# Optimization experiments

Measured on AMD Instinct MI355X. Metric: run time of the kernel, lower is better.

## Reference

```python
import jax, jax.numpy as jnp
import numpy as np
import math

V_RANGE = 1
SHIFTS = [(x, y) for x in range(-V_RANGE, V_RANGE + 1) for y in range(-V_RANGE, V_RANGE + 1)]


def circ_conv(x, w, b=None):
    # Conv2d with circular padding, NCHW / OIHW layout.
    p = w.shape[-1] // 2
    xp = jnp.pad(x, ((0, 0), (0, 0), (p, p), (p, p)), mode='wrap')
    y = jax.lax.conv_general_dilated(xp, w, (1, 1), 'VALID',
                                     dimension_numbers=('NCHW', 'OIHW', 'NCHW'))
    if b is not None:
        y = y + b[None, :, None, None]
    return y


def setup_inputs() -> dict:
    key = jax.random.key(0)
    ks = jax.random.split(key, 6)
    B, d_model, d_state, H, W = 4, 64, 16, 32, 32
    num_v = (2 * V_RANGE + 1) ** 2  # 9
    return {
        'u_t': jax.random.normal(ks[0], (B, d_model, H, W), jnp.float32),
        's_prev': jax.random.normal(ks[1], (B, num_v, d_model, d_state, H, W), jnp.float32),
        'W_delta': jax.random.normal(ks[2], (d_model, d_model, 3, 3), jnp.float32) * 0.05,
        'b_delta': jnp.zeros((d_model,), jnp.float32),
        'W_B': jax.random.normal(ks[3], (d_state, d_model, 3, 3), jnp.float32) * 0.05,
        'W_C': jax.random.normal(ks[4], (d_state, d_model, 3, 3), jnp.float32) * 0.05,
        'log_A_real': jnp.log(0.5 * jnp.ones((d_model, d_state), jnp.float32)),
        'D': jnp.ones((d_model,), jnp.float32),
        'dt_inv_softplus': jnp.float32(math.log(math.e - 1.0)),
    }


def reference(u_t, s_prev, W_delta, b_delta, W_B, W_C, log_A_real, D, dt_inv_softplus):
    # Parameter generation from input
    delta = jax.nn.softplus(circ_conv(u_t, W_delta, b_delta) + dt_inv_softplus)  # (B,d,H,W)
    B_val = circ_conv(u_t, W_B)  # (B,n,H,W)
    C_val = circ_conv(u_t, W_C)  # (B,n,H,W)

    # ZOH discretization (pointwise)
    A = -jnp.exp(log_A_real)                         # (d,n)
    A_bc = A[None, :, :, None, None]                 # (1,d,n,1,1)
    A_bar = jnp.exp(delta[:, :, None] * A_bc)        # (B,d,n,H,W)
    B_bar = (A_bar - 1.0) / A_bc * B_val[:, None]    # (B,d,n,H,W)
    bu = B_bar * u_t[:, :, None]                     # (B,d,n,H,W)

    # Transport: per-velocity spatial roll, vectorized with vmap over the V axis
    vx = jnp.array([s[0] for s in SHIFTS])
    vy = jnp.array([s[1] for s in SHIFTS])
    roll_v = jax.vmap(lambda s, x, y: jnp.roll(s, shift=(-y, -x), axis=(-2, -1)),
                      in_axes=(1, 0, 0), out_axes=1)
    s_trans = roll_v(s_prev, vx, vy)                 # (B,V,d,n,H,W)

    # State update and output
    s_next = A_bar[:, None] * s_trans + bu[:, None]  # (B,V,d,n,H,W)
    y_state = jnp.sum(s_next * C_val[:, None, None], axis=3)  # (B,V,d,H,W)
    y_out = y_state + (u_t * D[None, :, None, None])[:, None]
    return y_out, s_next
```

## Files before the change

kernel.cpp:

```cpp
#include <hip/hip_runtime.h>
#include <math.h>

#define B_   4
#define DM   64
#define DS   16
#define HW_  1024
#define NV   9

typedef float f32x4 __attribute__((ext_vector_type(4)));

#define Y_SIZE   2359296
#define WS_DELTA 0
#define WS_BV    (B_*DM*HW_)
#define WS_CV    (WS_BV + B_*DS*HW_)

__global__ __launch_bounds__(256) void conv_kernel(
    const float* __restrict__ u,
    const float* __restrict__ Wd,
    const float* __restrict__ bd,
    const float* __restrict__ Wb,
    const float* __restrict__ Wc,
    const float* __restrict__ dtp,
    float* __restrict__ ws)
{
    __shared__ float su[8 * 320];
    __shared__ float sw[DM * 9 * 4];

    const int bid = blockIdx.x;
    const int b   = bid / 96;
    const int r   = bid % 96;
    const int g   = r >> 2;
    const int h0  = (r & 3) * 8;
    const int co0 = g * 4;

    const float* Wsrc;
    int cbase, mode;
    if (co0 < 64)      { Wsrc = Wd; cbase = co0;      mode = 0; }
    else if (co0 < 80) { Wsrc = Wb; cbase = co0 - 64; mode = 1; }
    else               { Wsrc = Wc; cbase = co0 - 80; mode = 2; }

    const int tid = threadIdx.x;

    for (int i = tid; i < DM * 9 * 4; i += 256) {
        const int j  = i & 3;
        const int ct = i >> 2;
        sw[i] = Wsrc[(cbase + j) * 576 + ct];
    }

    const int hl = tid >> 5;
    const int w  = tid & 31;
    const int pix = ((h0 + hl) << 5) | w;

    float acc[4];
    #pragma unroll
    for (int j = 0; j < 4; ++j) acc[j] = 0.f;
    const float* ub = u + (size_t)b * DM * HW_;

    for (int c0 = 0; c0 < DM; c0 += 8) {
        __syncthreads();
        #pragma unroll
        for (int k = 0; k < 10; ++k) {
            const int i   = k * 256 + tid;
            const int cl  = i / 320;
            const int pos = i - cl * 320;
            const int rr  = pos >> 5;
            su[i] = ub[(c0 + cl) * HW_ + ((((h0 - 1 + rr) & 31) << 5) | (pos & 31))];
        }
        __syncthreads();
        #pragma unroll
        for (int cl = 0; cl < 8; ++cl) {
            #pragma unroll
            for (int kh = 0; kh < 3; ++kh) {
                const int rs = hl + kh;
                #pragma unroll
                for (int kw = 0; kw < 3; ++kw) {
                    const int ww = (w + kw + 31) & 31;
                    const float v = su[cl * 320 + ((rs << 5) | ww)];
                    const float4 w0 = *(const float4*)&sw[((c0 + cl) * 9 + kh * 3 + kw) * 4];
                    acc[0] = fmaf(v, w0.x, acc[0]);
                    acc[1] = fmaf(v, w0.y, acc[1]);
                    acc[2] = fmaf(v, w0.z, acc[2]);
                    acc[3] = fmaf(v, w0.w, acc[3]);
                }
            }
        }
    }

    if (mode == 0) {
        const float dt = dtp[0];
        #pragma unroll
        for (int j = 0; j < 4; ++j) {
            const float x  = acc[j] + bd[cbase + j] + dt;
            const float sp = fmaxf(x, 0.f) + log1pf(expf(-fabsf(x)));
            ws[WS_DELTA + ((size_t)b * DM + cbase + j) * HW_ + pix] = sp;
        }
    } else if (mode == 1) {
        #pragma unroll
        for (int j = 0; j < 4; ++j)
            ws[WS_BV + ((size_t)b * DS + cbase + j) * HW_ + pix] = acc[j];
    } else {
        #pragma unroll
        for (int j = 0; j < 4; ++j)
            ws[WS_CV + ((size_t)b * DS + cbase + j) * HW_ + pix] = acc[j];
    }
}

__global__ __launch_bounds__(512, 4) void scan_kernel(
    const float* __restrict__ u,
    const float* __restrict__ s_prev,
    const float* __restrict__ logA,
    const float* __restrict__ Dv,
    const float* __restrict__ ws,
    float* __restrict__ out)
{
    const int bid  = blockIdx.x >> 1;
    const int half = blockIdx.x & 1;
    const int c   = bid & 63;
    const int bv  = bid >> 6;
    const int v   = bv % 9;
    const int b   = bv / 9;

    __shared__ float sAr[DS], sIr[DS];
    __shared__ float syl[4 * 512];

    const int tid = threadIdx.x;
    if (tid < DS) {
        const float A = -__expf(logA[(c << 4) + tid]);
        sAr[tid] = A;
        sIr[tid] = 1.0f / A;
    }
    __syncthreads();

    const int quad = tid & 127;
    const int nthr = tid >> 7;
    const int lane = tid & 63;
    const int nb   = nthr << 2;

    const int hw4 = (half << 9) | (quad << 2);
    const int h   = hw4 >> 5;

    const int sx  = v / 3 - 1;
    const int syy = v % 3 - 1;
    const int hs  = (h + syy) & 31;
    const int rowbase = (hs << 5) | ((quad & 7) << 2);

    const int srcp = (lane & ~7) | ((lane + 1) & 7);
    const int srcm = (lane & ~7) | ((lane + 7) & 7);

    const int bc = (b << 6) | c;

    const float* __restrict__ sp  = s_prev + ((size_t)bid << 14);
    float* __restrict__ so        = out + Y_SIZE + ((size_t)bid << 14);
    const float* __restrict__ bvp = ws + WS_BV + ((b << 14) | hw4);
    const float* __restrict__ cvp = ws + WS_CV + ((b << 14) | hw4);

    float4 spv[4], bvv[4], cvv[4];
    #pragma unroll
    for (int i = 0; i < 4; ++i)
        spv[i] = *(const float4*)&sp[((nb + i) << 10) + rowbase];
    #pragma unroll
    for (int i = 0; i < 4; ++i) {
        bvv[i] = *(const float4*)&bvp[(nb + i) << 10];
        cvv[i] = *(const float4*)&cvp[(nb + i) << 10];
    }
    const float4 u4 = *(const float4*)&u[(bc << 10) | hw4];
    const float4 d4 = *(const float4*)&ws[WS_DELTA + ((bc << 10) | hw4)];

    float4 acc = make_float4(0.f, 0.f, 0.f, 0.f);
    #pragma unroll
    for (int i = 0; i < 4; ++i) {
        const int n = nb + i;
        float4 sh;
        if (sx > 0) {
            const float edge = __shfl(spv[i].x, srcp);
            sh = make_float4(spv[i].y, spv[i].z, spv[i].w, edge);
        } else if (sx < 0) {
            const float edge = __shfl(spv[i].w, srcm);
            sh = make_float4(edge, spv[i].x, spv[i].y, spv[i].z);
        } else {
            sh = spv[i];
        }
        const float A  = sAr[n];
        const float iA = sIr[n];
        float4 e;
        f32x4 s;
        e.x = __expf(d4.x * A);
        e.y = __expf(d4.y * A);
        e.z = __expf(d4.z * A);
        e.w = __expf(d4.w * A);
        s.x = fmaf(e.x, sh.x, (e.x - 1.f) * iA * bvv[i].x * u4.x);
        s.y = fmaf(e.y, sh.y, (e.y - 1.f) * iA * bvv[i].y * u4.y);
        s.z = fmaf(e.z, sh.z, (e.z - 1.f) * iA * bvv[i].z * u4.z);
        s.w = fmaf(e.w, sh.w, (e.w - 1.f) * iA * bvv[i].w * u4.w);
        __builtin_nontemporal_store(s, (f32x4*)&so[(n << 10) + hw4]);
        acc.x = fmaf(s.x, cvv[i].x, acc.x);
        acc.y = fmaf(s.y, cvv[i].y, acc.y);
        acc.z = fmaf(s.z, cvv[i].z, acc.z);
        acc.w = fmaf(s.w, cvv[i].w, acc.w);
    }

    *(float4*)&syl[(nthr << 9) | (quad << 2)] = make_float4(acc.x, acc.y, acc.z, acc.w);
    __syncthreads();
    if (tid < 128) {
        const float4 a0 = *(const float4*)&syl[(0 << 9) | (tid << 2)];
        const float4 a1 = *(const float4*)&syl[(1 << 9) | (tid << 2)];
        const float4 a2 = *(const float4*)&syl[(2 << 9) | (tid << 2)];
        const float4 a3 = *(const float4*)&syl[(3 << 9) | (tid << 2)];
        const float Dc = Dv[c];
        f32x4 y;
        y.x = a0.x + a1.x + a2.x + a3.x + u4.x * Dc;
        y.y = a0.y + a1.y + a2.y + a3.y + u4.y * Dc;
        y.z = a0.z + a1.z + a2.z + a3.z + u4.z * Dc;
        y.w = a0.w + a1.w + a2.w + a3.w + u4.w * Dc;
        __builtin_nontemporal_store(y, (f32x4*)&out[(bid << 10) | hw4]);
    }
}

extern "C" void kernel_launch(void* const* d_in, const int* in_sizes, int n_in,
                              void* d_out, int out_size, void* d_ws, size_t ws_size,
                              hipStream_t stream) {
    const float* u      = (const float*)d_in[0];
    const float* s_prev = (const float*)d_in[1];
    const float* Wd     = (const float*)d_in[2];
    const float* bd     = (const float*)d_in[3];
    const float* Wb     = (const float*)d_in[4];
    const float* Wc     = (const float*)d_in[5];
    const float* logA   = (const float*)d_in[6];
    const float* Dv     = (const float*)d_in[7];
    const float* dtp    = (const float*)d_in[8];
    float* out = (float*)d_out;
    float* ws  = (float*)d_ws;

    conv_kernel<<<B_ * 24 * 4, 256, 0, stream>>>(u, Wd, bd, Wb, Wc, dtp, ws);
    scan_kernel<<<B_ * NV * DM * 2, 512, 0, stream>>>(u, s_prev, logA, Dv, ws, out);
}
```

Before: 74.62 us.

## Make scan kernel persistent with software-prefetched s_prev tiles

```diff
diff --git a/kernel.cpp b/kernel.cpp
--- a/kernel.cpp
+++ b/kernel.cpp
@@ -13,6 +13,9 @@
 #define WS_DELTA 0
 #define WS_BV    (B_*DM*HW_)
 #define WS_CV    (WS_BV + B_*DS*HW_)
+
+#define NTILES   (B_*NV*DM*2)
+#define GRID_SCAN 512
 
 __global__ __launch_bounds__(256) void conv_kernel(
     const float* __restrict__ u,
@@ -113,106 +116,149 @@
     const float* __restrict__ ws,
     float* __restrict__ out)
 {
-    const int bid  = blockIdx.x >> 1;
-    const int half = blockIdx.x & 1;
-    const int c   = bid & 63;
-    const int bv  = bid >> 6;
-    const int v   = bv % 9;
-    const int b   = bv / 9;
-
-    __shared__ float sAr[DS], sIr[DS];
-    __shared__ float syl[4 * 512];
+    __shared__ float sA[DM * DS];
+    __shared__ float sI[DM * DS];
+    __shared__ float4 syl4[2][512];
 
     const int tid = threadIdx.x;
-    if (tid < DS) {
-        const float A = -__expf(logA[(c << 4) + tid]);
-        sAr[tid] = A;
-        sIr[tid] = 1.0f / A;
+
+    #pragma unroll
+    for (int k = 0; k < 2; ++k) {
+        const int i = (k << 9) | tid;
+        const float A = -__expf(logA[i]);
+        sA[i] = A;
+        sI[i] = 1.0f / A;
     }
     __syncthreads();
 
     const int quad = tid & 127;
     const int nthr = tid >> 7;
+    const int nb   = nthr << 2;
     const int lane = tid & 63;
-    const int nb   = nthr << 2;
-
-    const int hw4 = (half << 9) | (quad << 2);
-    const int h   = hw4 >> 5;
-
-    const int sx  = v / 3 - 1;
-    const int syy = v % 3 - 1;
-    const int hs  = (h + syy) & 31;
-    const int rowbase = (hs << 5) | ((quad & 7) << 2);
-
     const int srcp = (lane & ~7) | ((lane + 1) & 7);
     const int srcm = (lane & ~7) | ((lane + 7) & 7);
-
-    const int bc = (b << 6) | c;
-
-    const float* __restrict__ sp  = s_prev + ((size_t)bid << 14);
-    float* __restrict__ so        = out + Y_SIZE + ((size_t)bid << 14);
-    const float* __restrict__ bvp = ws + WS_BV + ((b << 14) | hw4);
-    const float* __restrict__ cvp = ws + WS_CV + ((b << 14) | hw4);
-
-    float4 spv[4], bvv[4], cvv[4];
-    #pragma unroll
-    for (int i = 0; i < 4; ++i)
-        spv[i] = *(const float4*)&sp[((nb + i) << 10) + rowbase];
-    #pragma unroll
-    for (int i = 0; i < 4; ++i) {
-        bvv[i] = *(const float4*)&bvp[(nb + i) << 10];
-        cvv[i] = *(const float4*)&cvp[(nb + i) << 10];
-    }
-    const float4 u4 = *(const float4*)&u[(bc << 10) | hw4];
-    const float4 d4 = *(const float4*)&ws[WS_DELTA + ((bc << 10) | hw4)];
-
-    float4 acc = make_float4(0.f, 0.f, 0.f, 0.f);
-    #pragma unroll
-    for (int i = 0; i < 4; ++i) {
-        const int n = nb + i;
-        float4 sh;
-        if (sx > 0) {
-            const float edge = __shfl(spv[i].x, srcp);
-            sh = make_float4(spv[i].y, spv[i].z, spv[i].w, edge);
-        } else if (sx < 0) {
-            const float edge = __shfl(spv[i].w, srcm);
-            sh = make_float4(edge, spv[i].x, spv[i].y, spv[i].z);
-        } else {
-            sh = spv[i];
-        }
-        const float A  = sAr[n];
-        const float iA = sIr[n];
-        float4 e;
-        f32x4 s;
-        e.x = __expf(d4.x * A);
-        e.y = __expf(d4.y * A);
-        e.z = __expf(d4.z * A);
-        e.w = __expf(d4.w * A);
-        s.x = fmaf(e.x, sh.x, (e.x - 1.f) * iA * bvv[i].x * u4.x);
-        s.y = fmaf(e.y, sh.y, (e.y - 1.f) * iA * bvv[i].y * u4.y);
-        s.z = fmaf(e.z, sh.z, (e.z - 1.f) * iA * bvv[i].z * u4.z);
-        s.w = fmaf(e.w, sh.w, (e.w - 1.f) * iA * bvv[i].w * u4.w);
-        __builtin_nontemporal_store(s, (f32x4*)&so[(n << 10) + hw4]);
-        acc.x = fmaf(s.x, cvv[i].x, acc.x);
-        acc.y = fmaf(s.y, cvv[i].y, acc.y);
-        acc.z = fmaf(s.z, cvv[i].z, acc.z);
-        acc.w = fmaf(s.w, cvv[i].w, acc.w);
-    }
-
-    *(float4*)&syl[(nthr << 9) | (quad << 2)] = make_float4(acc.x, acc.y, acc.z, acc.w);
-    __syncthreads();
-    if (tid < 128) {
-        const float4 a0 = *(const float4*)&syl[(0 << 9) | (tid << 2)];
-        const float4 a1 = *(const float4*)&syl[(1 << 9) | (tid << 2)];
-        const float4 a2 = *(const float4*)&syl[(2 << 9) | (tid << 2)];
-        const float4 a3 = *(const float4*)&syl[(3 << 9) | (tid << 2)];
-        const float Dc = Dv[c];
-        f32x4 y;
-        y.x = a0.x + a1.x + a2.x + a3.x + u4.x * Dc;
-        y.y = a0.y + a1.y + a2.y + a3.y + u4.y * Dc;
-        y.z = a0.z + a1.z + a2.z + a3.z + u4.z * Dc;
-        y.w = a0.w + a1.w + a2.w + a3.w + u4.w * Dc;
-        __builtin_nontemporal_store(y, (f32x4*)&out[(bid << 10) | hw4]);
+    const int colb = (quad & 7) << 2;
+    const int qw   = quad << 2;
+
+    int tile = blockIdx.x;
+    int bid  = tile >> 1;
+    int c    = bid & 63;
+    int b, sx;
+    {
+        const int bv = bid >> 6;
+        const int v  = bv % 9;
+        b  = bv / 9;
+        sx = v / 3 - 1;
+        const int syy = v % 3 - 1;
+        const int hw4_ = ((tile & 1) << 9) | qw;
+        const int hs = ((hw4_ >> 5) + syy) & 31;
+        (void)hs;
+    }
+    int hw4 = ((tile & 1) << 9) | qw;
+    float4 spv[4];
+    {
+        const int bv = bid >> 6;
+        const int v  = bv % 9;
+        const int syy = v % 3 - 1;
+        const int hs = ((hw4 >> 5) + syy) & 31;
+        const int rowbase = (hs << 5) | colb;
+        const float* sp = s_prev + ((size_t)bid << 14);
+        #pragma unroll
+        for (int i = 0; i < 4; ++i)
+            spv[i] = *(const float4*)&sp[((nb + i) << 10) + rowbase];
+    }
+
+    int p = 0;
+    for (;;) {
+        const int bc = (b << 6) | c;
+        const float4 u4 = *(const float4*)&u[(bc << 10) | hw4];
+        const float4 d4 = *(const float4*)&ws[WS_DELTA + ((bc << 10) | hw4)];
+        const float* __restrict__ bvp = ws + WS_BV + ((b << 14) | hw4);
+        const float* __restrict__ cvp = ws + WS_CV + ((b << 14) | hw4);
+        float4 bvv[4], cvv[4];
+        #pragma unroll
+        for (int i = 0; i < 4; ++i) {
+            bvv[i] = *(const float4*)&bvp[(nb + i) << 10];
+            cvv[i] = *(const float4*)&cvp[(nb + i) << 10];
+        }
+
+        const int ntile = tile + GRID_SCAN;
+        const bool have_next = ntile < NTILES;
+        int nbid = 0, nc = 0, nb2 = 0, nsx = 0, nhw4 = 0;
+        float4 spn[4];
+        if (have_next) {
+            nbid = ntile >> 1;
+            nc   = nbid & 63;
+            const int nbv = nbid >> 6;
+            const int nv  = nbv % 9;
+            nb2  = nbv / 9;
+            nsx  = nv / 3 - 1;
+            const int nsy = nv % 3 - 1;
+            nhw4 = ((ntile & 1) << 9) | qw;
+            const int nhs = ((nhw4 >> 5) + nsy) & 31;
+            const int nrow = (nhs << 5) | colb;
+            const float* nsp = s_prev + ((size_t)nbid << 14);
+            #pragma unroll
+            for (int i = 0; i < 4; ++i)
+                spn[i] = *(const float4*)&nsp[((nb + i) << 10) + nrow];
+        }
+
+        float* __restrict__ so = out + Y_SIZE + ((size_t)bid << 14);
+        float4 acc = make_float4(0.f, 0.f, 0.f, 0.f);
+        #pragma unroll
+        for (int i = 0; i < 4; ++i) {
+            const int n = nb + i;
+            float4 sh;
+            if (sx > 0) {
+                const float edge = __shfl(spv[i].x, srcp);
+                sh = make_float4(spv[i].y, spv[i].z, spv[i].w, edge);
+            } else if (sx < 0) {
+                const float edge = __shfl(spv[i].w, srcm);
+                sh = make_float4(edge, spv[i].x, spv[i].y, spv[i].z);
+            } else {
+                sh = spv[i];
+            }
+            const float A  = sA[(c << 4) + n];
+            const float iA = sI[(c << 4) + n];
+            float4 e;
+            f32x4 s;
+            e.x = __expf(d4.x * A);
+            e.y = __expf(d4.y * A);
+            e.z = __expf(d4.z * A);
+            e.w = __expf(d4.w * A);
+            s.x = fmaf(e.x, sh.x, (e.x - 1.f) * iA * bvv[i].x * u4.x);
+            s.y = fmaf(e.y, sh.y, (e.y - 1.f) * iA * bvv[i].y * u4.y);
+            s.z = fmaf(e.z, sh.z, (e.z - 1.f) * iA * bvv[i].z * u4.z);
+            s.w = fmaf(e.w, sh.w, (e.w - 1.f) * iA * bvv[i].w * u4.w);
+            __builtin_nontemporal_store(s, (f32x4*)&so[(n << 10) + hw4]);
+            acc.x = fmaf(s.x, cvv[i].x, acc.x);
+            acc.y = fmaf(s.y, cvv[i].y, acc.y);
+            acc.z = fmaf(s.z, cvv[i].z, acc.z);
+            acc.w = fmaf(s.w, cvv[i].w, acc.w);
+        }
+
+        syl4[p][(nthr << 7) | quad] = acc;
+        asm volatile("s_waitcnt lgkmcnt(0)" ::: "memory");
+        __builtin_amdgcn_s_barrier();
+        if (tid < 128) {
+            const float4 a0 = syl4[p][(0 << 7) | tid];
+            const float4 a1 = syl4[p][(1 << 7) | tid];
+            const float4 a2 = syl4[p][(2 << 7) | tid];
+            const float4 a3 = syl4[p][(3 << 7) | tid];
+            const float Dc = Dv[c];
+            f32x4 y;
+            y.x = a0.x + a1.x + a2.x + a3.x + u4.x * Dc;
+            y.y = a0.y + a1.y + a2.y + a3.y + u4.y * Dc;
+            y.z = a0.z + a1.z + a2.z + a3.z + u4.z * Dc;
+            y.w = a0.w + a1.w + a2.w + a3.w + u4.w * Dc;
+            __builtin_nontemporal_store(y, (f32x4*)&out[(bid << 10) | hw4]);
+        }
+
+        if (!have_next) break;
+        tile = ntile; bid = nbid; c = nc; b = nb2; sx = nsx; hw4 = nhw4;
+        #pragma unroll
+        for (int i = 0; i < 4; ++i) spv[i] = spn[i];
+        p ^= 1;
     }
 }
 
@@ -232,5 +278,5 @@
     float* ws  = (float*)d_ws;
 
     conv_kernel<<<B_ * 24 * 4, 256, 0, stream>>>(u, Wd, bd, Wb, Wc, dtp, ws);
-    scan_kernel<<<B_ * NV * DM * 2, 512, 0, stream>>>(u, s_prev, logA, Dv, ws, out);
+    scan_kernel<<<GRID_SCAN, 512, 0, stream>>>(u, s_prev, logA, Dv, ws, out);
 }
```

Result: slower. 76.22 us (+2.1%).
